# Kernel optimization log

Hardware: AMD Instinct MI355X
Metric: run time of the kernel (lower is better)

The kernel has to match this reference:

```python
import jax, jax.numpy as jnp
import numpy as np


def setup_inputs() -> dict:
    key = jax.random.key(0)
    ks = jax.random.split(key, 8)
    B, T, D, H, HD = 4, 2048, 1024, 16, 64
    s = 0.02
    return {
        "x": jax.random.normal(ks[0], (B, T, D), dtype=jnp.float32),
        "Wq": jax.random.normal(ks[1], (H, D, HD), dtype=jnp.float32) * s,
        "bq": jnp.zeros((H, HD), dtype=jnp.float32),
        "Wk": jax.random.normal(ks[2], (H, D, HD), dtype=jnp.float32) * s,
        "bk": jnp.zeros((H, HD), dtype=jnp.float32),
        "Wv": jax.random.normal(ks[3], (H, D, HD), dtype=jnp.float32) * s,
        "bv": jnp.zeros((H, HD), dtype=jnp.float32),
        "Wo": jax.random.normal(ks[4], (D, D), dtype=jnp.float32) * s,
        "bo": jnp.zeros((D,), dtype=jnp.float32),
        "mask": 1,
    }


def reference(x, Wq, bq, Wk, bk, Wv, bv, Wo, bo, mask):
    B, T, D = x.shape
    # stacked per-head projections: [B,H,T,hd]
    q = jnp.einsum('btd,hde->bhte', x, Wq) + bq[None, :, None, :]
    k = jnp.einsum('btd,hde->bhte', x, Wk) + bk[None, :, None, :]
    v = jnp.einsum('btd,hde->bhte', x, Wv) + bv[None, :, None, :]
    hd = q.shape[-1]
    # FAITHFUL to source: scores = QK^T / hd**(-0.5) == QK^T * sqrt(hd)
    scores = jnp.einsum('bhte,bhse->bhts', q, k) * (float(hd) ** 0.5)
    if mask:
        causal = jnp.tril(jnp.ones((T, T), dtype=bool))
        scores = jnp.where(causal[None, None, :, :], scores, -jnp.inf)
    att = jax.nn.softmax(scores, axis=-1)  # dropout is identity in eval
    out = jnp.einsum('bhts,bhse->bhte', att, v)
    # concat heads along feature dim (head order matches ModuleList order)
    out = out.transpose(0, 2, 1, 3).reshape(B, T, D)
    return out @ Wo + bo
```

## Files before the change

### kernel.cpp

```cpp
#include <hip/hip_runtime.h>
#include <hip/hip_bf16.h>
#include <math.h>

#define B_  4
#define T_  2048
#define D_  1024
#define H_  16
#define HD_ 64
#define M_  8192

typedef __attribute__((ext_vector_type(8))) _Float16 f16x8;
typedef __attribute__((ext_vector_type(4))) float   f32x4;

static __device__ __forceinline__ unsigned short f2h(float f){
    union { _Float16 h; unsigned short u; } cv; cv.h = (_Float16)f; return cv.u;
}
static __device__ __forceinline__ void gload_lds16(const void* g, void* l){
    __builtin_amdgcn_global_load_lds(
        (const __attribute__((address_space(1))) unsigned int*)g,
        (__attribute__((address_space(3))) unsigned int*)l, 16, 0, 0);
}

union U16x16 { unsigned short us[16]; uint4 q[2]; };
union U16x4  { unsigned short us[4];  uint2 q;    };

__global__ __launch_bounds__(256) void prep_xh(
    const float* __restrict__ x, unsigned short* __restrict__ xb)
{
    const size_t i = ((size_t)blockIdx.x*256 + threadIdx.x)*16;
    U16x16 u;
#pragma unroll
    for (int j=0;j<16;j+=4){
        float4 f = *(const float4*)(x+i+j);
        u.us[j+0]=f2h(f.x); u.us[j+1]=f2h(f.y);
        u.us[j+2]=f2h(f.z); u.us[j+3]=f2h(f.w);
    }
    *(uint4*)(xb+i)   = u.q[0];
    *(uint4*)(xb+i+8) = u.q[1];
}

__global__ __launch_bounds__(256) void prep_wqkvh(
    const float* __restrict__ Wq, const float* __restrict__ Wk,
    const float* __restrict__ Wv, unsigned short* __restrict__ wt)
{
    const int dt = blockIdx.x;
    const int zh = blockIdx.y;
    const int z = zh >> 4, h = zh & 15;
    const float* src = ((z==0)?Wq:(z==1)?Wk:Wv) + (size_t)h*1024*64;
    __shared__ float Tt[64][68];
    const int t = threadIdx.x;
    const int r = t >> 2, c4 = (t & 3) * 16;
    const float* sp = src + (size_t)(dt*64 + r)*64 + c4;
    float4 v0=*(const float4*)(sp+0), v1=*(const float4*)(sp+4);
    float4 v2=*(const float4*)(sp+8), v3=*(const float4*)(sp+12);
    *(float4*)&Tt[r][c4+ 0]=v0; *(float4*)&Tt[r][c4+ 4]=v1;
    *(float4*)&Tt[r][c4+ 8]=v2; *(float4*)&Tt[r][c4+12]=v3;
    __syncthreads();
    const int er = t >> 2, dk = (t & 3) * 16;
    U16x16 u;
#pragma unroll
    for (int j=0;j<16;j++) u.us[j] = f2h(Tt[dk+j][er]);
    unsigned short* dst = wt + (size_t)(z*1024 + h*64 + er)*1024 + dt*64 + dk;
    *(uint4*)(dst)   = u.q[0];
    *(uint4*)(dst+8) = u.q[1];
}

__global__ __launch_bounds__(256) void prep_woh(
    const float* __restrict__ Wo, unsigned short* __restrict__ wot)
{
    const int kt = blockIdx.x, nt = blockIdx.y;
    __shared__ float Tt[64][68];
    const int t = threadIdx.x;
    const int r = t >> 2, c4 = (t & 3) * 16;
    const float* sp = Wo + (size_t)(kt*64 + r)*1024 + nt*64 + c4;
    float4 v0=*(const float4*)(sp+0), v1=*(const float4*)(sp+4);
    float4 v2=*(const float4*)(sp+8), v3=*(const float4*)(sp+12);
    *(float4*)&Tt[r][c4+ 0]=v0; *(float4*)&Tt[r][c4+ 4]=v1;
    *(float4*)&Tt[r][c4+ 8]=v2; *(float4*)&Tt[r][c4+12]=v3;
    __syncthreads();
    const int er = t >> 2, dk = (t & 3) * 16;
    U16x16 u;
#pragma unroll
    for (int j=0;j<16;j++) u.us[j] = f2h(Tt[dk+j][er]);
    unsigned short* dst = wot + (size_t)(nt*64 + er)*1024 + kt*64 + dk;
    *(uint4*)(dst)   = u.q[0];
    *(uint4*)(dst+8) = u.q[1];
}

__global__ __launch_bounds__(256) void gemm_qkvh(
    const unsigned short* __restrict__ xb, const unsigned short* __restrict__ wt,
    const float* __restrict__ bqv, const float* __restrict__ bkv,
    const float* __restrict__ bvv,
    unsigned short* __restrict__ qp, unsigned short* __restrict__ kp,
    unsigned short* __restrict__ vtp)
{
    const int m0 = blockIdx.x * 128;
    const int n0 = blockIdx.y * 128;
    const int tid = threadIdx.x;
    const int lane = tid & 63, w = tid >> 6;
    const int wr = w >> 1, wc = w & 1;
    const int fla = lane & 15, flb = lane >> 4;

    __shared__ unsigned short As[128*32];
    __shared__ unsigned short Bs[128*32];

    f32x4 acc[4][4];
#pragma unroll
    for (int i=0;i<4;i++)
#pragma unroll
        for (int j=0;j<4;j++) acc[i][j] = (f32x4){0.f,0.f,0.f,0.f};

    const int srow0 = w*32 + (lane>>2);
    const int srow1 = srow0 + 16;
    const int spc   = lane & 3;
    const size_t ga0 = (size_t)(m0+srow0)*1024 + (size_t)((spc ^ ((srow0>>1)&3))*8);
    const size_t ga1 = (size_t)(m0+srow1)*1024 + (size_t)((spc ^ ((srow1>>1)&3))*8);
    const size_t gb0 = (size_t)(n0+srow0)*1024 + (size_t)((spc ^ ((srow0>>1)&3))*8);
    const size_t gb1 = (size_t)(n0+srow1)*1024 + (size_t)((spc ^ ((srow1>>1)&3))*8);
    const int ldso0 = w*1024;
    const int ldso1 = w*1024 + 512;
    const int pchunk = (flb ^ ((fla>>1)&3)) * 8;

    for (int ks = 0; ks < 32; ++ks){
        const size_t k0 = (size_t)ks*32;
        __syncthreads();
        gload_lds16(xb + ga0 + k0, As + ldso0);
        gload_lds16(xb + ga1 + k0, As + ldso1);
        gload_lds16(wt + gb0 + k0, Bs + ldso0);
        gload_lds16(wt + gb1 + k0, Bs + ldso1);
        __syncthreads();

        f16x8 af[4], bfr[4];
#pragma unroll
        for (int mf=0; mf<4; ++mf)
            af[mf] = *(const f16x8*)&As[(wr*64+mf*16+fla)*32 + pchunk];
#pragma unroll
        for (int nf=0; nf<4; ++nf)
            bfr[nf] = *(const f16x8*)&Bs[(wc*64+nf*16+fla)*32 + pchunk];
#pragma unroll
        for (int mf=0; mf<4; ++mf)
#pragma unroll
            for (int nf=0; nf<4; ++nf)
                acc[mf][nf] = __builtin_amdgcn_mfma_f32_16x16x32_f16(
                                  af[mf], bfr[nf], acc[mf][nf], 0, 0, 0);
    }

#pragma unroll
    for (int nf=0; nf<4; ++nf){
        const int c = n0 + wc*64 + nf*16 + fla;
        const int z = c >> 10, rem = c & 1023;
        const int h = rem >> 6, e = rem & 63;
        if (z < 2){
            const float bias = ((z==0)?bqv:bkv)[rem];
            const float scl  = (z==0) ? 8.0f : 1.0f;
            unsigned short* op = (z==0)?qp:kp;
#pragma unroll
            for (int mf=0; mf<4; ++mf){
#pragma unroll
                for (int ri=0; ri<4; ++ri){
                    const int m = m0 + wr*64 + mf*16 + flb*4 + ri;
                    const int b = m >> 11, t = m & (T_-1);
                    op[((size_t)(b*H_ + h)*T_ + t)*HD_ + e] =
                        f2h((acc[mf][nf][ri] + bias) * scl);
                }
            }
        } else {
            const float bias = bvv[rem];
#pragma unroll
            for (int mf=0; mf<4; ++mf){
                const int m = m0 + wr*64 + mf*16 + flb*4;
                const int b = m >> 11, t = m & (T_-1);
                U16x4 u;
#pragma unroll
                for (int ri=0; ri<4; ++ri)
                    u.us[ri] = f2h(acc[mf][nf][ri] + bias);
                *(uint2*)(vtp + ((size_t)(b*H_ + h)*HD_ + e)*T_ + t) = u.q;
            }
        }
    }
}

__global__ __launch_bounds__(256) void gemm_o(
    const unsigned short* __restrict__ attb, const unsigned short* __restrict__ wot,
    const float* __restrict__ bo, float* __restrict__ out)
{
    const int m0 = blockIdx.x * 128;
    const int n0 = blockIdx.y * 128;
    const int tid = threadIdx.x;
    const int lane = tid & 63, w = tid >> 6;
    const int wr = w >> 1, wc = w & 1;
    const int fla = lane & 15, flb = lane >> 4;

    __shared__ unsigned short As[4096];
    __shared__ unsigned short Bs[4096];

    f32x4 acc[4][4];
#pragma unroll
    for (int i=0;i<4;i++)
#pragma unroll
        for (int j=0;j<4;j++) acc[i][j] = (f32x4){0.f,0.f,0.f,0.f};

    const int srow0 = w*32 + (lane>>2);
    const int srow1 = srow0 + 16;
    const int spc   = lane & 3;
    const size_t ga0 = (size_t)(m0+srow0)*1024 + (size_t)((spc ^ ((srow0>>1)&3))*8);
    const size_t ga1 = (size_t)(m0+srow1)*1024 + (size_t)((spc ^ ((srow1>>1)&3))*8);
    const size_t gb0 = (size_t)(n0+srow0)*1024 + (size_t)((spc ^ ((srow0>>1)&3))*8);
    const size_t gb1 = (size_t)(n0+srow1)*1024 + (size_t)((spc ^ ((srow1>>1)&3))*8);
    const int ldso0 = w*1024;
    const int ldso1 = w*1024 + 512;
    const int pchunk = (flb ^ ((fla>>1)&3)) * 8;

    for (int ks = 0; ks < 32; ++ks){
        const size_t k0 = (size_t)ks*32;
        __syncthreads();
        gload_lds16(attb + ga0 + k0, As + ldso0);
        gload_lds16(attb + ga1 + k0, As + ldso1);
        gload_lds16(wot  + gb0 + k0, Bs + ldso0);
        gload_lds16(wot  + gb1 + k0, Bs + ldso1);
        __syncthreads();

        f16x8 af[4], bfr[4];
#pragma unroll
        for (int mf=0; mf<4; ++mf)
            af[mf] = *(const f16x8*)&As[(wr*64+mf*16+fla)*32 + pchunk];
#pragma unroll
        for (int nf=0; nf<4; ++nf)
            bfr[nf] = *(const f16x8*)&Bs[(wc*64+nf*16+fla)*32 + pchunk];
#pragma unroll
        for (int mf=0; mf<4; ++mf)
#pragma unroll
            for (int nf=0; nf<4; ++nf)
                acc[mf][nf] = __builtin_amdgcn_mfma_f32_16x16x32_f16(
                                  af[mf], bfr[nf], acc[mf][nf], 0, 0, 0);
    }

#pragma unroll
    for (int nf=0; nf<4; ++nf){
        const int n = n0 + wc*64 + nf*16 + fla;
        const float bias = bo[n];
#pragma unroll
        for (int mf=0; mf<4; ++mf){
#pragma unroll
            for (int ri=0; ri<4; ++ri){
                const int m = m0 + wr*64 + mf*16 + flb*4 + ri;
                out[(size_t)m*D_ + n] = acc[mf][nf][ri] + bias;
            }
        }
    }
}

__global__ __launch_bounds__(256) void attn_mfma(
    const unsigned short* __restrict__ qp, const unsigned short* __restrict__ kp,
    const unsigned short* __restrict__ vtp, unsigned short* __restrict__ attb,
    const int* __restrict__ maskp)
{
    const int bid = blockIdx.x;
    const int qb  = 31 - (bid >> 6);
    const int bh  = bid & 63;
    const int b   = bh >> 4, h = bh & 15;
    const int tid = threadIdx.x;
    const int lane = tid & 63, w = tid >> 6;
    const int l16 = lane & 15, h16 = lane >> 4;
    const int domask = maskp[0];

    __shared__ unsigned short KS [64][72];
    __shared__ unsigned short VtS[64][72];
    __shared__ unsigned short PsS[64][72];

    const int qrow = qb*64 + w*16 + l16;
    const size_t qoff = ((size_t)bh*T_ + qrow)*HD_ + 8*h16;
    const f16x8 q0 = *(const f16x8*)(qp + qoff);
    const f16x8 q1 = *(const f16x8*)(qp + qoff + 32);

    f32x4 accO[4];
#pragma unroll
    for (int j=0;j<4;j++) accO[j] = (f32x4){0.f,0.f,0.f,0.f};
    float m_run[4], l_run[4];
#pragma unroll
    for (int i=0;i<4;i++){ m_run[i] = -INFINITY; l_run[i] = 0.f; }

    const int r   = tid >> 2;
    const int c16 = (tid & 3) * 16;
    const size_t kbase = (size_t)bh*T_*HD_;
    const size_t vbase = (size_t)bh*HD_*T_;

    const int kv_end = domask ? qb : 31;
    for (int kv = 0; kv <= kv_end; ++kv){
        const unsigned short* ksrc = kp + kbase + (size_t)(kv*64+r)*HD_ + c16;
        uint4 a0 = *(const uint4*)(ksrc);
        uint4 a1 = *(const uint4*)(ksrc+8);
        const unsigned short* vsrc = vtp + vbase + (size_t)r*T_ + kv*64 + c16;
        uint4 a4 = *(const uint4*)(vsrc);
        uint4 a5 = *(const uint4*)(vsrc+8);
        __syncthreads();
        *(uint4*)&KS [r][c16] = a0; *(uint4*)&KS [r][c16+8] = a1;
        *(uint4*)&VtS[r][c16] = a4; *(uint4*)&VtS[r][c16+8] = a5;
        __syncthreads();

        f32x4 s[4];
#pragma unroll
        for (int j=0;j<4;j++){
            const f16x8 k0 = *(const f16x8*)&KS[j*16+l16][8*h16];
            const f16x8 k1 = *(const f16x8*)&KS[j*16+l16][32+8*h16];
            f32x4 a = (f32x4){0.f,0.f,0.f,0.f};
            a = __builtin_amdgcn_mfma_f32_16x16x32_f16(q0, k0, a, 0,0,0);
            a = __builtin_amdgcn_mfma_f32_16x16x32_f16(q1, k1, a, 0,0,0);
            s[j] = a;
        }
        if (domask && kv == qb){
#pragma unroll
            for (int j=0;j<4;j++)
#pragma unroll
                for (int reg=0;reg<4;reg++)
                    if (j*16+l16 > w*16 + h16*4 + reg) s[j][reg] = -INFINITY;
        }

#pragma unroll
        for (int reg=0; reg<4; ++reg){
            float mloc = fmaxf(fmaxf(s[0][reg],s[1][reg]), fmaxf(s[2][reg],s[3][reg]));
            mloc = fmaxf(mloc, __shfl_xor(mloc,1));
            mloc = fmaxf(mloc, __shfl_xor(mloc,2));
            mloc = fmaxf(mloc, __shfl_xor(mloc,4));
            mloc = fmaxf(mloc, __shfl_xor(mloc,8));
            float mnew = fmaxf(m_run[reg], mloc);
            float scl  = __expf(m_run[reg] - mnew);
            m_run[reg] = mnew;
            float p0 = __expf(s[0][reg]-mnew);
            float p1 = __expf(s[1][reg]-mnew);
            float p2 = __expf(s[2][reg]-mnew);
            float p3 = __expf(s[3][reg]-mnew);
            float rs = p0+p1+p2+p3;
            rs += __shfl_xor(rs,1); rs += __shfl_xor(rs,2);
            rs += __shfl_xor(rs,4); rs += __shfl_xor(rs,8);
            l_run[reg] = l_run[reg]*scl + rs;
            accO[0][reg] *= scl; accO[1][reg] *= scl;
            accO[2][reg] *= scl; accO[3][reg] *= scl;
            const int prow = w*16 + h16*4 + reg;
            PsS[prow][ 0+l16] = f2h(p0);
            PsS[prow][16+l16] = f2h(p1);
            PsS[prow][32+l16] = f2h(p2);
            PsS[prow][48+l16] = f2h(p3);
        }

#pragma unroll
        for (int c=0;c<2;c++){
            const f16x8 pa = *(const f16x8*)&PsS[w*16+l16][c*32+8*h16];
#pragma unroll
            for (int j=0;j<4;j++){
                const f16x8 vb_ = *(const f16x8*)&VtS[j*16+l16][c*32+8*h16];
                accO[j] = __builtin_amdgcn_mfma_f32_16x16x32_f16(pa, vb_, accO[j], 0,0,0);
            }
        }
    }

#pragma unroll
    for (int reg=0;reg<4;reg++){
        const float inv = 1.0f / l_run[reg];
        const int t = qb*64 + w*16 + h16*4 + reg;
#pragma unroll
        for (int j=0;j<4;j++){
            attb[((size_t)b*T_ + t)*D_ + h*HD_ + j*16 + l16] =
                f2h(accO[j][reg]*inv);
        }
    }
}

extern "C" void kernel_launch(void* const* d_in, const int* in_sizes, int n_in,
                              void* d_out, int out_size, void* d_ws, size_t ws_size,
                              hipStream_t stream)
{
    const float* x  = (const float*)d_in[0];
    const float* Wq = (const float*)d_in[1];
    const float* bq = (const float*)d_in[2];
    const float* Wk = (const float*)d_in[3];
    const float* bk = (const float*)d_in[4];
    const float* Wv = (const float*)d_in[5];
    const float* bv = (const float*)d_in[6];
    const float* Wo = (const float*)d_in[7];
    const float* bo = (const float*)d_in[8];
    const int* mask = (const int*)d_in[9];
    float* out = (float*)d_out;

    unsigned short* qp  = (unsigned short*)d_ws;
    unsigned short* kp  = qp  + (size_t)8*1024*1024;
    unsigned short* vtp = kp  + (size_t)8*1024*1024;
    unsigned short* xb  = vtp + (size_t)8*1024*1024;
    unsigned short* wt  = xb  + (size_t)8*1024*1024;
    unsigned short* wot = wt  + (size_t)3*1024*1024;
    unsigned short* attb = xb;

    prep_xh   <<<2048, 256, 0, stream>>>(x, xb);
    prep_wqkvh<<<dim3(16,48), 256, 0, stream>>>(Wq, Wk, Wv, wt);
    prep_woh  <<<dim3(16,16), 256, 0, stream>>>(Wo, wot);
    gemm_qkvh <<<dim3(64,24), 256, 0, stream>>>(xb, wt, bq, bk, bv, qp, kp, vtp);
    attn_mfma <<<2048, 256, 0, stream>>>(qp, kp, vtp, attb, mask);
    gemm_o    <<<dim3(64,8), 256, 0, stream>>>(attb, wot, bo, out);
}
```

Before: 215.4 us.

## Use exp2 with log2e-folded Q scale, lazy rescaling, and swizzled LDS layout

Folds log2(e) into the Q projection scale so the softmax can use exp2f in place of __expf. It adds lazy rescaling: the running max and accumulators are only updated when some row's tile max exceeds the running max by more than a threshold, checked wave-wide. It also replaces the padded LDS arrays with XOR-swizzled, half-split tiles to avoid bank conflicts while using less shared memory. The lazy rescale lets unnormalised probabilities grow by up to about 2^8 before rescaling, which narrows fp16 headroom for P.

```diff
diff --git a/kernel.cpp b/kernel.cpp
--- a/kernel.cpp
+++ b/kernel.cpp
@@ -152,7 +152,8 @@
         const int h = rem >> 6, e = rem & 63;
         if (z < 2){
             const float bias = ((z==0)?bqv:bkv)[rem];
-            const float scl  = (z==0) ? 8.0f : 1.0f;
+            const float scl  = (z==0) ? 11.541560327111708f
+                                      : 1.0f;
             unsigned short* op = (z==0)?qp:kp;
 #pragma unroll
             for (int mf=0; mf<4; ++mf){
@@ -264,9 +265,9 @@
     const int l16 = lane & 15, h16 = lane >> 4;
     const int domask = maskp[0];
 
-    __shared__ unsigned short KS [64][72];
-    __shared__ unsigned short VtS[64][72];
-    __shared__ unsigned short PsS[64][72];
+    __shared__ unsigned short KS [2][64][32];
+    __shared__ unsigned short VtS[2][64][32];
+    __shared__ unsigned short PsS[2][64][32];
 
     const int qrow = qb*64 + w*16 + l16;
     const size_t qoff = ((size_t)bh*T_ + qrow)*HD_ + 8*h16;
@@ -281,7 +282,16 @@
     for (int i=0;i<4;i++){ m_run[i] = -INFINITY; l_run[i] = 0.f; }
 
     const int r   = tid >> 2;
-    const int c16 = (tid & 3) * 16;
+    const int cq  = tid & 3;
+    const int sci = cq >> 1;
+    const int sb0 = (cq & 1) * 2;
+    const int fr  = (r >> 1) & 3;
+    const int sd0 = ((sb0  ) ^ fr)*8;
+    const int sd1 = ((sb0+1) ^ fr)*8;
+    const int c16 = cq * 16;
+
+    const int off = (h16 ^ ((l16>>1)&3)) * 8;
+
     const size_t kbase = (size_t)bh*T_*HD_;
     const size_t vbase = (size_t)bh*HD_*T_;
 
@@ -294,15 +304,15 @@
         uint4 a4 = *(const uint4*)(vsrc);
         uint4 a5 = *(const uint4*)(vsrc+8);
         __syncthreads();
-        *(uint4*)&KS [r][c16] = a0; *(uint4*)&KS [r][c16+8] = a1;
-        *(uint4*)&VtS[r][c16] = a4; *(uint4*)&VtS[r][c16+8] = a5;
+        *(uint4*)&KS [sci][r][sd0] = a0; *(uint4*)&KS [sci][r][sd1] = a1;
+        *(uint4*)&VtS[sci][r][sd0] = a4; *(uint4*)&VtS[sci][r][sd1] = a5;
         __syncthreads();
 
         f32x4 s[4];
 #pragma unroll
         for (int j=0;j<4;j++){
-            const f16x8 k0 = *(const f16x8*)&KS[j*16+l16][8*h16];
-            const f16x8 k1 = *(const f16x8*)&KS[j*16+l16][32+8*h16];
+            const f16x8 k0 = *(const f16x8*)&KS[0][j*16+l16][off];
+            const f16x8 k1 = *(const f16x8*)&KS[1][j*16+l16][off];
             f32x4 a = (f32x4){0.f,0.f,0.f,0.f};
             a = __builtin_amdgcn_mfma_f32_16x16x32_f16(q0, k0, a, 0,0,0);
             a = __builtin_amdgcn_mfma_f32_16x16x32_f16(q1, k1, a, 0,0,0);
@@ -316,6 +326,7 @@
                     if (j*16+l16 > w*16 + h16*4 + reg) s[j][reg] = -INFINITY;
         }
 
+        float pmax[4];
 #pragma unroll
         for (int reg=0; reg<4; ++reg){
             float mloc = fmaxf(fmaxf(s[0][reg],s[1][reg]), fmaxf(s[2][reg],s[3][reg]));
@@ -323,32 +334,47 @@
             mloc = fmaxf(mloc, __shfl_xor(mloc,2));
             mloc = fmaxf(mloc, __shfl_xor(mloc,4));
             mloc = fmaxf(mloc, __shfl_xor(mloc,8));
-            float mnew = fmaxf(m_run[reg], mloc);
-            float scl  = __expf(m_run[reg] - mnew);
-            m_run[reg] = mnew;
-            float p0 = __expf(s[0][reg]-mnew);
-            float p1 = __expf(s[1][reg]-mnew);
-            float p2 = __expf(s[2][reg]-mnew);
-            float p3 = __expf(s[3][reg]-mnew);
+            pmax[reg] = mloc;
+        }
+        const bool small = (pmax[0] <= m_run[0]+8.f) && (pmax[1] <= m_run[1]+8.f)
+                        && (pmax[2] <= m_run[2]+8.f) && (pmax[3] <= m_run[3]+8.f);
+        if (!__all(small)){
+#pragma unroll
+            for (int reg=0; reg<4; ++reg){
+                const float mnew = fmaxf(m_run[reg], pmax[reg]);
+                const float scl  = exp2f(m_run[reg] - mnew);
+                m_run[reg] = mnew;
+                l_run[reg] *= scl;
+                accO[0][reg] *= scl; accO[1][reg] *= scl;
+                accO[2][reg] *= scl; accO[3][reg] *= scl;
+            }
+        }
+        const int sbl = l16 >> 3, pos = l16 & 7;
+#pragma unroll
+        for (int reg=0; reg<4; ++reg){
+            const float mr = m_run[reg];
+            float p0 = exp2f(s[0][reg]-mr);
+            float p1 = exp2f(s[1][reg]-mr);
+            float p2 = exp2f(s[2][reg]-mr);
+            float p3 = exp2f(s[3][reg]-mr);
             float rs = p0+p1+p2+p3;
             rs += __shfl_xor(rs,1); rs += __shfl_xor(rs,2);
             rs += __shfl_xor(rs,4); rs += __shfl_xor(rs,8);
-            l_run[reg] = l_run[reg]*scl + rs;
-            accO[0][reg] *= scl; accO[1][reg] *= scl;
-            accO[2][reg] *= scl; accO[3][reg] *= scl;
+            l_run[reg] += rs;
             const int prow = w*16 + h16*4 + reg;
-            PsS[prow][ 0+l16] = f2h(p0);
-            PsS[prow][16+l16] = f2h(p1);
-            PsS[prow][32+l16] = f2h(p2);
-            PsS[prow][48+l16] = f2h(p3);
+            const int psw  = (prow>>1)&3;
+            PsS[0][prow][((sbl  ) ^ psw)*8 + pos] = f2h(p0);
+            PsS[0][prow][((sbl+2) ^ psw)*8 + pos] = f2h(p1);
+            PsS[1][prow][((sbl  ) ^ psw)*8 + pos] = f2h(p2);
+            PsS[1][prow][((sbl+2) ^ psw)*8 + pos] = f2h(p3);
         }
 
 #pragma unroll
         for (int c=0;c<2;c++){
-            const f16x8 pa = *(const f16x8*)&PsS[w*16+l16][c*32+8*h16];
+            const f16x8 pa = *(const f16x8*)&PsS[c][w*16+l16][off];
 #pragma unroll
             for (int j=0;j<4;j++){
-                const f16x8 vb_ = *(const f16x8*)&VtS[j*16+l16][c*32+8*h16];
+                const f16x8 vb_ = *(const f16x8*)&VtS[c][j*16+l16][off];
                 accO[j] = __builtin_amdgcn_mfma_f32_16x16x32_f16(pa, vb_, accO[j], 0,0,0);
             }
         }
```

Result: no change. 215.2 us (-0.1%).
